# Performance work log

Hardware: AMD Instinct MI355X
Metric: run time of the kernel (lower is better)

The kernel has to match this reference:

```python
import jax, jax.numpy as jnp
import numpy as np

TEMPERATURE = 0.1
NSAMPLE = 32
B, N_PER, M_PER, C_FEAT = 2, 16384, 4096, 64


def setup_inputs() -> dict:
    key = jax.random.key(0)
    ks = jax.random.split(key, 4)
    xyz = jax.random.normal(ks[0], (B * N_PER, 3), jnp.float32)
    new_xyz = jax.random.normal(ks[1], (B * M_PER, 3), jnp.float32)
    new_xyz_r = jax.random.uniform(ks[2], (B * M_PER, 1), jnp.float32, minval=0.5, maxval=1.0)
    features = jax.random.normal(ks[3], (B * N_PER, C_FEAT), jnp.float32)
    xyz_batch_cnt = jnp.full((B,), N_PER, jnp.int32)
    new_xyz_batch_cnt = jnp.full((B,), M_PER, jnp.int32)
    temperature_decay = jnp.ones((1,), jnp.float32)
    return dict(xyz=xyz, xyz_batch_cnt=xyz_batch_cnt, new_xyz=new_xyz,
                new_xyz_r=new_xyz_r, new_xyz_batch_cnt=new_xyz_batch_cnt,
                features=features, temperature_decay=temperature_decay)


def _ball_query(xyz_b, new_xyz_b, r_b, nsample):
    # xyz_b: (B,N,3), new_xyz_b: (B,M,3), r_b: (B,M)
    # Returns idx (B,M,nsample) int32 (batch-local point indices, first-in-order
    # within the ball, remaining slots filled with first hit, 0 if empty) and
    # empty mask (B,M) bool. Mirrors the CUDA ball_query_deform kernel.
    N = xyz_b.shape[1]
    d2 = jnp.sum((new_xyz_b[:, :, None, :] - xyz_b[:, None, :, :]) ** 2, axis=-1)  # (B,M,N)
    within = d2 < (r_b ** 2)[..., None]
    # key = point index if within radius else N; top_k of -key gives the first
    # nsample in-ball indices in ascending index order.
    key = jnp.where(within, jnp.arange(N, dtype=jnp.int32), jnp.int32(N))
    neg_vals, _ = jax.lax.top_k(-key, nsample)
    cand = -neg_vals  # (B,M,nsample)
    cnt = within.sum(axis=-1)  # (B,M)
    slot_valid = jnp.arange(nsample) < cnt[..., None]
    idx = jnp.where(slot_valid, cand, cand[..., :1])  # pad with first found index
    empty = cnt == 0
    idx = jnp.where(empty[..., None], 0, idx)
    return idx.astype(jnp.int32), empty


def reference(xyz, xyz_batch_cnt, new_xyz, new_xyz_r, new_xyz_batch_cnt, features, temperature_decay):
    b = xyz_batch_cnt.shape[0]
    n = xyz.shape[0] // b
    m = new_xyz.shape[0] // b
    c = features.shape[1]
    real_t = TEMPERATURE * temperature_decay[0]
    explore_r = new_xyz_r + real_t * 5.0  # (M_tot, 1)

    xyz_b = xyz.reshape(b, n, 3)
    nxyz_b = new_xyz.reshape(b, m, 3)
    idx_b, empty_b = _ball_query(xyz_b, nxyz_b, explore_r.reshape(b, m), NSAMPLE)

    gather = jax.vmap(lambda pts, i: pts[i])  # per-batch gather

    grouped_xyz = gather(xyz_b, idx_b)                 # (B,M,ns,3)
    grouped_xyz = grouped_xyz - nxyz_b[:, :, None, :]  # center
    grouped_xyz = jnp.where(empty_b[:, :, None, None], 0.0, grouped_xyz)
    grouped_xyz = grouped_xyz.reshape(b * m, NSAMPLE, 3).transpose(0, 2, 1)  # (M_tot,3,ns)

    dist_xyz = jnp.sqrt(jnp.sum(grouped_xyz * grouped_xyz, axis=1))  # (M_tot,ns)
    weights = 1.0 - jax.nn.sigmoid((dist_xyz - new_xyz_r) / real_t)  # (M_tot,ns)

    feat_b = features.reshape(b, n, c)
    grouped_feat = gather(feat_b, idx_b)  # (B,M,ns,C)
    grouped_feat = jnp.where(empty_b[:, :, None, None], 0.0, grouped_feat)
    grouped_feat = grouped_feat.reshape(b * m, NSAMPLE, c).transpose(0, 2, 1)  # (M_tot,C,ns)

    new_features = jnp.concatenate([grouped_xyz, grouped_feat], axis=1)  # (M_tot,3+C,ns)
    idx = idx_b.reshape(b * m, NSAMPLE)
    return new_features, weights, idx
```

## Files before the change

### kernel.cpp

```cpp
#include <hip/hip_runtime.h>
#include <math.h>

#define NS 32
#define WPB 4
#define SCAN0 2048
#define TSTRIDE 36

__device__ __forceinline__ void write_query(
    int m, int bb, bool empty, int lane,
    const int* sIdxW, float* sT,
    const float* __restrict__ xyz, const float* __restrict__ new_xyz,
    const float* __restrict__ new_xyz_r, const float* __restrict__ features,
    float real_t, float* __restrict__ out, int N_per, int C, int M_tot)
{
#pragma clang fp contract(off)
    const float* xb = xyz + (size_t)bb * N_per * 3;
    const int    j  = lane & 31;
    const size_t nf_base = (size_t)m * (3 + C) * NS;
    float* wout = out + (size_t)M_tot * (3 + C) * NS;
    float* iout = wout + (size_t)M_tot * NS;

    if (lane < NS) {
        const float qx = new_xyz[(size_t)m * 3 + 0];
        const float qy = new_xyz[(size_t)m * 3 + 1];
        const float qz = new_xyz[(size_t)m * 3 + 2];
        const float r_orig = new_xyz_r[m];
        const int pj = empty ? 0 : sIdxW[j];
        float gx = 0.f, gy = 0.f, gz = 0.f;
        if (!empty) {
            gx = xb[(size_t)pj * 3 + 0] - qx;
            gy = xb[(size_t)pj * 3 + 1] - qy;
            gz = xb[(size_t)pj * 3 + 2] - qz;
        }
        float d2 = gx * gx;
        d2 = d2 + gy * gy;
        d2 = d2 + gz * gz;
        float dist = sqrtf(d2);
        float wt = 1.0f / (1.0f + expf((dist - r_orig) / real_t));
        out[nf_base + 0 * NS + j] = gx;
        out[nf_base + 1 * NS + j] = gy;
        out[nf_base + 2 * NS + j] = gz;
        wout[(size_t)m * NS + j] = wt;
        iout[(size_t)m * NS + j] = (float)pj;
    }

    const float* fb = features + (size_t)bb * N_per * C;
    int c0 = 0;
    for (; c0 + 32 <= C; c0 += 32) {
        const int k  = lane & 7;
        const int f4 = 4 * (k & 3);
        #pragma unroll
        for (int t = 0; t < 4; ++t) {
            const int r  = 8 * t + (lane >> 3);
            const int pj = empty ? 0 : sIdxW[r];
            float4 v = make_float4(0.f, 0.f, 0.f, 0.f);
            if (!empty) v = *(const float4*)(fb + (size_t)pj * C + c0 + 4 * k);
            const int rs = r ^ f4;
            sT[(4 * k + 0) * TSTRIDE + rs] = v.x;
            sT[(4 * k + 1) * TSTRIDE + rs] = v.y;
            sT[(4 * k + 2) * TSTRIDE + rs] = v.z;
            sT[(4 * k + 3) * TSTRIDE + rs] = v.w;
        }
        const int jg = lane & 7;
        #pragma unroll
        for (int s2 = 0; s2 < 4; ++s2) {
            const int ch = 8 * s2 + (lane >> 3);
            const int jb = (4 * jg) ^ (4 * ((ch >> 2) & 3));
            float4 w = *(const float4*)&sT[ch * TSTRIDE + jb];
            *(float4*)&out[nf_base + (size_t)(3 + c0 + ch) * NS + 4 * jg] = w;
        }
    }
    if (c0 < C) {
        const int h  = lane >> 5;
        const int pj = empty ? 0 : sIdxW[j];
        const float* frow = fb + (size_t)pj * C;
        for (int c = c0 + h; c < C; c += 2) {
            float v = empty ? 0.f : frow[c];
            out[nf_base + (size_t)(3 + c) * NS + j] = v;
        }
    }
}

__device__ __forceinline__ void write_query_coop(
    int m, int bb, bool empty, int lane, int wv,
    const int* sIdxW, float* sT,
    const float* __restrict__ xyz, const float* __restrict__ new_xyz,
    const float* __restrict__ new_xyz_r, const float* __restrict__ features,
    float real_t, float* __restrict__ out, int N_per, int C, int M_tot)
{
#pragma clang fp contract(off)
    const size_t nf_base = (size_t)m * (3 + C) * NS;

    if (wv == 3) {
        const float* xb = xyz + (size_t)bb * N_per * 3;
        const int    j  = lane & 31;
        float* wout = out + (size_t)M_tot * (3 + C) * NS;
        float* iout = wout + (size_t)M_tot * NS;
        if (lane < NS) {
            const float qx = new_xyz[(size_t)m * 3 + 0];
            const float qy = new_xyz[(size_t)m * 3 + 1];
            const float qz = new_xyz[(size_t)m * 3 + 2];
            const float r_orig = new_xyz_r[m];
            const int pj = empty ? 0 : sIdxW[j];
            float gx = 0.f, gy = 0.f, gz = 0.f;
            if (!empty) {
                gx = xb[(size_t)pj * 3 + 0] - qx;
                gy = xb[(size_t)pj * 3 + 1] - qy;
                gz = xb[(size_t)pj * 3 + 2] - qz;
            }
            float d2 = gx * gx;
            d2 = d2 + gy * gy;
            d2 = d2 + gz * gz;
            float dist = sqrtf(d2);
            float wt = 1.0f / (1.0f + expf((dist - r_orig) / real_t));
            out[nf_base + 0 * NS + j] = gx;
            out[nf_base + 1 * NS + j] = gy;
            out[nf_base + 2 * NS + j] = gz;
            wout[(size_t)m * NS + j] = wt;
            iout[(size_t)m * NS + j] = (float)pj;
        }
        const int c0f = (C / 32) * 32;
        if (c0f < C) {
            const int h  = lane >> 5;
            const int pj = empty ? 0 : sIdxW[j];
            const float* frow = features + (size_t)bb * N_per * C + (size_t)pj * C;
            for (int c = c0f + h; c < C; c += 2) {
                float v = empty ? 0.f : frow[c];
                out[nf_base + (size_t)(3 + c) * NS + j] = v;
            }
        }
        return;
    }

    const float* fb = features + (size_t)bb * N_per * C;
    for (int c0 = 32 * wv; c0 + 32 <= C; c0 += 96) {
        const int k  = lane & 7;
        const int f4 = 4 * (k & 3);
        #pragma unroll
        for (int t = 0; t < 4; ++t) {
            const int r  = 8 * t + (lane >> 3);
            const int pj = empty ? 0 : sIdxW[r];
            float4 v = make_float4(0.f, 0.f, 0.f, 0.f);
            if (!empty) v = *(const float4*)(fb + (size_t)pj * C + c0 + 4 * k);
            const int rs = r ^ f4;
            sT[(4 * k + 0) * TSTRIDE + rs] = v.x;
            sT[(4 * k + 1) * TSTRIDE + rs] = v.y;
            sT[(4 * k + 2) * TSTRIDE + rs] = v.z;
            sT[(4 * k + 3) * TSTRIDE + rs] = v.w;
        }
        const int jg = lane & 7;
        #pragma unroll
        for (int s2 = 0; s2 < 4; ++s2) {
            const int ch = 8 * s2 + (lane >> 3);
            const int jb = (4 * jg) ^ (4 * ((ch >> 2) & 3));
            float4 w = *(const float4*)&sT[ch * TSTRIDE + jb];
            *(float4*)&out[nf_base + (size_t)(3 + c0 + ch) * NS + 4 * jg] = w;
        }
    }
}

__device__ __forceinline__ int scan_range(
    const float* __restrict__ xb, float qx, float qy, float qz, float er2,
    int rb, int re, int lane, unsigned long long lt, int* hits)
{
#pragma clang fp contract(off)
    int cnt = 0;
    for (int base = rb; base < re; base += 256) {
        float d2k[4];
        #pragma unroll
        for (int k = 0; k < 4; ++k) {
            int p = base + k * 64 + lane;
            int pc = (p < re) ? p : (re - 1);
            const float* pp = xb + (size_t)pc * 3;
            float dx = pp[0] - qx, dy = pp[1] - qy, dz = pp[2] - qz;
            float d2 = dx * dx;
            d2 = d2 + dy * dy;
            d2 = d2 + dz * dz;
            d2k[k] = (p < re) ? d2 : 1e30f;
        }
        #pragma unroll
        for (int k = 0; k < 4; ++k) {
            bool hit = d2k[k] < er2;
            unsigned long long msk = __ballot(hit);
            if (hit) {
                int slot = cnt + (int)__popcll(msk & lt);
                if (slot < NS) hits[slot] = base + k * 64 + lane;
            }
            cnt += (int)__popcll(msk);
        }
        if (cnt >= NS) break;
    }
    return cnt;
}

__device__ __forceinline__ int scan_range_deep(
    const float* __restrict__ xb, float qx, float qy, float qz, float er2,
    int rb, int re, int lane, unsigned long long lt, int* hits)
{
#pragma clang fp contract(off)
    int cnt = 0;
    for (int base = rb; base < re; base += 512) {
        float d2k[8];
        #pragma unroll
        for (int k = 0; k < 8; ++k) {
            int p = base + k * 64 + lane;
            int pc = (p < re) ? p : (re - 1);
            const float* pp = xb + (size_t)pc * 3;
            float dx = pp[0] - qx, dy = pp[1] - qy, dz = pp[2] - qz;
            float d2 = dx * dx;
            d2 = d2 + dy * dy;
            d2 = d2 + dz * dz;
            d2k[k] = (p < re) ? d2 : 1e30f;
        }
        #pragma unroll
        for (int k = 0; k < 8; ++k) {
            bool hit = d2k[k] < er2;
            unsigned long long msk = __ballot(hit);
            if (hit) {
                int slot = cnt + (int)__popcll(msk & lt);
                if (slot < NS) hits[slot] = base + k * 64 + lane;
            }
            cnt += (int)__popcll(msk);
        }
        if (cnt >= NS) break;
    }
    return cnt;
}

__global__ __launch_bounds__(256) void qgd_F(
    const float* __restrict__ xyz, const float* __restrict__ new_xyz,
    const float* __restrict__ new_xyz_r, const float* __restrict__ features,
    const float* __restrict__ tdec, float* __restrict__ out,
    int N_per, int M_per, int C, int M_tot)
{
#pragma clang fp contract(off)
    __shared__ __align__(16) float sBuf[WPB * 32 * TSTRIDE];
    __shared__ int sIdx[WPB][NS];
    __shared__ int sH[WPB][NS];
    __shared__ int sCnt[WPB];
    __shared__ int sStrag[WPB];
    __shared__ int sC[WPB];
    __shared__ int sM[NS];
    __shared__ int sTot;

    const int lane = threadIdx.x & 63;
    const int wv   = threadIdx.x >> 6;
    const int m    = blockIdx.x * WPB + wv;
    const bool valid = (m < M_tot);

    const float real_t = 0.1f * tdec[0];
    const unsigned long long lt = (1ull << lane) - 1ull;
    const int scan0 = (SCAN0 < N_per) ? SCAN0 : N_per;

    int cnt = 0;
    int bb = 0;
    if (valid) {
        bb = m / M_per;
        const float* xb = xyz + (size_t)bb * N_per * 3;
        const float qx = new_xyz[(size_t)m * 3 + 0];
        const float qy = new_xyz[(size_t)m * 3 + 1];
        const float qz = new_xyz[(size_t)m * 3 + 2];
        const float er  = new_xyz_r[m] + real_t * 5.0f;
        const float er2 = er * er;

        cnt = scan_range(xb, qx, qy, qz, er2, 0, scan0, lane, lt, sIdx[wv]);

        if (cnt >= NS) {
            write_query(m, bb, false, lane, sIdx[wv],
                        sBuf + wv * (32 * TSTRIDE),
                        xyz, new_xyz, new_xyz_r, features, real_t, out,
                        N_per, C, M_tot);
        }
    }
    if (lane == 0) {
        sCnt[wv]   = cnt;
        sStrag[wv] = (valid && cnt < NS) ? 1 : 0;
    }
    __syncthreads();

    for (int s = 0; s < WPB; ++s) {
        if (!sStrag[s]) continue;

        const int ms  = blockIdx.x * WPB + s;
        const int bbs = ms / M_per;
        const float* xbs = xyz + (size_t)bbs * N_per * 3;
        const float qx = new_xyz[(size_t)ms * 3 + 0];
        const float qy = new_xyz[(size_t)ms * 3 + 1];
        const float qz = new_xyz[(size_t)ms * 3 + 2];
        const float er  = new_xyz_r[ms] + real_t * 5.0f;
        const float er2 = er * er;

        const int rem = N_per - scan0;
        const int rb  = scan0 + (int)(((long long)rem * wv) / WPB);
        const int re  = scan0 + (int)(((long long)rem * (wv + 1)) / WPB);

        int c2 = scan_range_deep(xbs, qx, qy, qz, er2, rb, re, lane, lt, sH[wv]);
        if (lane == 0) sC[wv] = (c2 < NS) ? c2 : NS;
        __syncthreads();

        if (threadIdx.x < NS) {
            const int j  = threadIdx.x;
            const int cp = sCnt[s];
            const int c0 = sC[0], c1 = sC[1], c2_ = sC[2], c3 = sC[3];
            const int o0 = cp, o1 = o0 + c0, o2 = o1 + c1, o3 = o2 + c2_;
            const int tot = o3 + c3;
            int v = 0;
            if (j < tot) {
                if      (j <  o0) v = sIdx[s][j];
                else if (j <  o1) v = sH[0][j - o0];
                else if (j <  o2) v = sH[1][j - o1];
                else if (j <  o3) v = sH[2][j - o2];
                else              v = sH[3][j - o3];
            }
            int first = 0;
            if      (cp  > 0) first = sIdx[s][0];
            else if (c0  > 0) first = sH[0][0];
            else if (c1  > 0) first = sH[1][0];
            else if (c2_ > 0) first = sH[2][0];
            else if (c3  > 0) first = sH[3][0];
            sM[j] = (tot == 0) ? 0 : ((j < tot) ? v : first);
            if (j == 0) sTot = tot;
        }
        __syncthreads();

        write_query_coop(ms, bbs, (sTot == 0), lane, wv, sM,
                         sBuf + wv * (32 * TSTRIDE),
                         xyz, new_xyz, new_xyz_r, features, real_t, out,
                         N_per, C, M_tot);
        __syncthreads();
    }
}

extern "C" void kernel_launch(void* const* d_in, const int* in_sizes, int n_in,
                              void* d_out, int out_size, void* d_ws, size_t ws_size,
                              hipStream_t stream) {
    const float* xyz       = (const float*)d_in[0];
    const float* new_xyz   = (const float*)d_in[2];
    const float* new_xyz_r = (const float*)d_in[3];
    const float* features  = (const float*)d_in[5];
    const float* tdec      = (const float*)d_in[6];

    const int B     = in_sizes[1];
    const int N_tot = in_sizes[0] / 3;
    const int M_tot = in_sizes[2] / 3;
    const int C     = in_sizes[5] / N_tot;
    const int N_per = N_tot / B;
    const int M_per = M_tot / B;

    float* out = (float*)d_out;

    const int blocks = (M_tot + WPB - 1) / WPB;
    qgd_F<<<blocks, 256, 0, stream>>>(xyz, new_xyz, new_xyz_r, features,
                                      tdec, out, N_per, M_per, C, M_tot);
}
```

Baseline: 118.4 us.

## Split straggler queries into a compacted second kernel with global work list

The fused kernel becomes two passes. The first kernel scans the first 2048 points per query and writes finished queries directly. Queries that still have fewer than 32 hits are appended to a global list via an atomic counter. A second kernel with a fixed 2048-block grid then processes only those stragglers, each block splitting the full point range across 4 waves. The aim is to stop blocks idling while a few waves chase stragglers, and to balance deep scans across the GPU. The cost is an extra launch, a memset, atomics, and rescanning the first 2048 points for each straggler.

```diff
diff --git a/kernel.cpp b/kernel.cpp
--- a/kernel.cpp
+++ b/kernel.cpp
@@ -227,94 +227,97 @@
     return cnt;
 }
 
-__global__ __launch_bounds__(256) void qgd_F(
+__global__ __launch_bounds__(256) void qgd_A(
     const float* __restrict__ xyz, const float* __restrict__ new_xyz,
     const float* __restrict__ new_xyz_r, const float* __restrict__ features,
     const float* __restrict__ tdec, float* __restrict__ out,
+    int* __restrict__ counter, int* __restrict__ list,
     int N_per, int M_per, int C, int M_tot)
 {
 #pragma clang fp contract(off)
     __shared__ __align__(16) float sBuf[WPB * 32 * TSTRIDE];
     __shared__ int sIdx[WPB][NS];
+
+    const int lane = threadIdx.x & 63;
+    const int wv   = threadIdx.x >> 6;
+    const int m    = blockIdx.x * WPB + wv;
+    if (m >= M_tot) return;
+
+    const int bb = m / M_per;
+    const float* xb = xyz + (size_t)bb * N_per * 3;
+    const float qx = new_xyz[(size_t)m * 3 + 0];
+    const float qy = new_xyz[(size_t)m * 3 + 1];
+    const float qz = new_xyz[(size_t)m * 3 + 2];
+    const float real_t = 0.1f * tdec[0];
+    const float er  = new_xyz_r[m] + real_t * 5.0f;
+    const float er2 = er * er;
+    const unsigned long long lt = (1ull << lane) - 1ull;
+    const int scan0 = (SCAN0 < N_per) ? SCAN0 : N_per;
+
+    int cnt = scan_range(xb, qx, qy, qz, er2, 0, scan0, lane, lt, sIdx[wv]);
+
+    if (cnt >= NS) {
+        write_query(m, bb, false, lane, sIdx[wv],
+                    sBuf + wv * (32 * TSTRIDE),
+                    xyz, new_xyz, new_xyz_r, features, real_t, out,
+                    N_per, C, M_tot);
+    } else if (lane == 0) {
+        int pos = atomicAdd(counter, 1);
+        atomicExch(&list[pos], m);
+    }
+}
+
+__global__ __launch_bounds__(256) void qgd_B(
+    const float* __restrict__ xyz, const float* __restrict__ new_xyz,
+    const float* __restrict__ new_xyz_r, const float* __restrict__ features,
+    const float* __restrict__ tdec, float* __restrict__ out,
+    const int* __restrict__ counter, const int* __restrict__ list,
+    int N_per, int M_per, int C, int M_tot)
+{
+#pragma clang fp contract(off)
+    __shared__ __align__(16) float sBuf[WPB * 32 * TSTRIDE];
     __shared__ int sH[WPB][NS];
-    __shared__ int sCnt[WPB];
-    __shared__ int sStrag[WPB];
     __shared__ int sC[WPB];
     __shared__ int sM[NS];
     __shared__ int sTot;
 
     const int lane = threadIdx.x & 63;
     const int wv   = threadIdx.x >> 6;
-    const int m    = blockIdx.x * WPB + wv;
-    const bool valid = (m < M_tot);
-
+    const int nstrag = *counter;
+    const unsigned long long lt = (1ull << lane) - 1ull;
     const float real_t = 0.1f * tdec[0];
-    const unsigned long long lt = (1ull << lane) - 1ull;
-    const int scan0 = (SCAN0 < N_per) ? SCAN0 : N_per;
-
-    int cnt = 0;
-    int bb = 0;
-    if (valid) {
-        bb = m / M_per;
-        const float* xb = xyz + (size_t)bb * N_per * 3;
-        const float qx = new_xyz[(size_t)m * 3 + 0];
-        const float qy = new_xyz[(size_t)m * 3 + 1];
-        const float qz = new_xyz[(size_t)m * 3 + 2];
-        const float er  = new_xyz_r[m] + real_t * 5.0f;
+
+    for (int it = blockIdx.x; it < nstrag; it += gridDim.x) {
+        const int mq  = list[it];
+        const int bbs = mq / M_per;
+        const float* xbs = xyz + (size_t)bbs * N_per * 3;
+        const float qx = new_xyz[(size_t)mq * 3 + 0];
+        const float qy = new_xyz[(size_t)mq * 3 + 1];
+        const float qz = new_xyz[(size_t)mq * 3 + 2];
+        const float er  = new_xyz_r[mq] + real_t * 5.0f;
         const float er2 = er * er;
 
-        cnt = scan_range(xb, qx, qy, qz, er2, 0, scan0, lane, lt, sIdx[wv]);
-
-        if (cnt >= NS) {
-            write_query(m, bb, false, lane, sIdx[wv],
-                        sBuf + wv * (32 * TSTRIDE),
-                        xyz, new_xyz, new_xyz_r, features, real_t, out,
-                        N_per, C, M_tot);
-        }
-    }
-    if (lane == 0) {
-        sCnt[wv]   = cnt;
-        sStrag[wv] = (valid && cnt < NS) ? 1 : 0;
-    }
-    __syncthreads();
-
-    for (int s = 0; s < WPB; ++s) {
-        if (!sStrag[s]) continue;
-
-        const int ms  = blockIdx.x * WPB + s;
-        const int bbs = ms / M_per;
-        const float* xbs = xyz + (size_t)bbs * N_per * 3;
-        const float qx = new_xyz[(size_t)ms * 3 + 0];
-        const float qy = new_xyz[(size_t)ms * 3 + 1];
-        const float qz = new_xyz[(size_t)ms * 3 + 2];
-        const float er  = new_xyz_r[ms] + real_t * 5.0f;
-        const float er2 = er * er;
-
-        const int rem = N_per - scan0;
-        const int rb  = scan0 + (int)(((long long)rem * wv) / WPB);
-        const int re  = scan0 + (int)(((long long)rem * (wv + 1)) / WPB);
-
-        int c2 = scan_range_deep(xbs, qx, qy, qz, er2, rb, re, lane, lt, sH[wv]);
+        const int rb = (int)(((long long)N_per * wv) / WPB);
+        const int re = (int)(((long long)N_per * (wv + 1)) / WPB);
+        int c2 = scan_range_deep(xbs, qx, qy, qz, er2, rb, re, lane, lt,
+                                 sH[wv]);
         if (lane == 0) sC[wv] = (c2 < NS) ? c2 : NS;
         __syncthreads();
 
         if (threadIdx.x < NS) {
             const int j  = threadIdx.x;
-            const int cp = sCnt[s];
             const int c0 = sC[0], c1 = sC[1], c2_ = sC[2], c3 = sC[3];
-            const int o0 = cp, o1 = o0 + c0, o2 = o1 + c1, o3 = o2 + c2_;
+            const int o1 = c0, o2 = c0 + c1, o3 = o2 + c2_;
             const int tot = o3 + c3;
             int v = 0;
             if (j < tot) {
-                if      (j <  o0) v = sIdx[s][j];
-                else if (j <  o1) v = sH[0][j - o0];
-                else if (j <  o2) v = sH[1][j - o1];
-                else if (j <  o3) v = sH[2][j - o2];
-                else              v = sH[3][j - o3];
+                if      (j >= o3) v = sH[3][j - o3];
+                else if (j >= o2) v = sH[2][j - o2];
+                else if (j >= o1) v = sH[1][j - o1];
+                else              v = sH[0][j];
             }
             int first = 0;
-            if      (cp  > 0) first = sIdx[s][0];
-            else if (c0  > 0) first = sH[0][0];
+            if      (c0  > 0) first = sH[0][0];
             else if (c1  > 0) first = sH[1][0];
             else if (c2_ > 0) first = sH[2][0];
             else if (c3  > 0) first = sH[3][0];
@@ -323,7 +326,7 @@
         }
         __syncthreads();
 
-        write_query_coop(ms, bbs, (sTot == 0), lane, wv, sM,
+        write_query_coop(mq, bbs, (sTot == 0), lane, wv, sM,
                          sBuf + wv * (32 * TSTRIDE),
                          xyz, new_xyz, new_xyz_r, features, real_t, out,
                          N_per, C, M_tot);
@@ -347,9 +350,17 @@
     const int N_per = N_tot / B;
     const int M_per = M_tot / B;
 
-    float* out = (float*)d_out;
-
-    const int blocks = (M_tot + WPB - 1) / WPB;
-    qgd_F<<<blocks, 256, 0, stream>>>(xyz, new_xyz, new_xyz_r, features,
-                                      tdec, out, N_per, M_per, C, M_tot);
-}
+    float* out     = (float*)d_out;
+    int*   counter = (int*)d_ws;
+    int*   list    = (int*)d_ws + 4;
+
+    hipMemsetAsync(counter, 0, sizeof(int), stream);
+
+    const int blocksA = (M_tot + WPB - 1) / WPB;
+    qgd_A<<<blocksA, 256, 0, stream>>>(xyz, new_xyz, new_xyz_r, features,
+                                       tdec, out, counter, list,
+                                       N_per, M_per, C, M_tot);
+    qgd_B<<<2048, 256, 0, stream>>>(xyz, new_xyz, new_xyz_r, features,
+                                    tdec, out, counter, list,
+                                    N_per, M_per, C, M_tot);
+}
```

Result: faster. 115.7 us (-2.3%).
